# Optimization experiments

Hardware: AMD Instinct MI355X
Metric: run time of the kernel (lower is better)

Reference implementation:

```python
import jax, jax.numpy as jnp
import numpy as np

B = 1048576  # batch size
D = 16       # in_dim == hid_dim == out_dim (required by the torch matmul broadcasting)


def setup_inputs() -> dict:
    key = jax.random.key(0)
    kx, kw = jax.random.split(key)
    x = jax.random.normal(kx, (B, D), dtype=jnp.float32)
    W = jax.random.normal(kw, (D, D, D), dtype=jnp.float32) * (1.0 / D)
    return {"x": x, "W": W}


def reference(x, W):
    # Original torch: xBx = x @ W @ x.T permuted, then take the batch diagonal.
    # Mathematically: out[b, k] = sum_{i, j} x[b, i] * W[k, i, j] * x[b, j]
    # (batched bilinear/quadratic form per output channel k). We compute only
    # the needed diagonal terms instead of the full BxB cross-batch product.
    return jnp.einsum('bi,kij,bj->bk', x, W, x)
```

## Files before the change

kernel.cpp:

```cpp
#include <hip/hip_runtime.h>
#include <hip/hip_bf16.h>


typedef __attribute__((ext_vector_type(8)))  short  short8;
typedef __attribute__((ext_vector_type(8)))  __bf16 bf16x8;
typedef __attribute__((ext_vector_type(4)))  float  floatx4;

#define DEV static __device__ __forceinline__

constexpr int cA(int c) {
    if (c < 24) { const int dIdx = c >> 1, v = c & 1;
        const int hi = dIdx / 3, lo = dIdx % 3 + 1;
        const int base = (hi == 3) ? 1 : 0;
        const int l = v ? ((lo == 1) ? 2 : 1) : 0;
        return base * 4 + l; }
    if (c < 36) { const int g = c - 24, hi = g / 4 + 1, l = g & 3;
        const int base = (hi == 3) ? 1 : 0;
        return base * 4 + l; }
    return c - 36;
}
constexpr int cDd(int c) {
    if (c < 24) { const int dIdx = c >> 1;
        return (dIdx / 3) * 4 + (dIdx % 3 + 1); }
    if (c < 36) { return ((c - 24) / 4 + 1) * 4; }
    return 0;
}
constexpr int   cB(int c) { return cA(c) ^ cDd(c); }
constexpr float cW(int c) { return (c >= 24 && c < 36) ? 0.5f : 1.0f; }

template <int C>
DEV float pval(const float* xv) {
    return xv[cA(C)] * xv[cB(C)];
}

template <int S>
DEV short8 make_afrag(const float* xv) {
    union { short8 s; __hip_bfloat162 h[4]; } u;
    u.h[0] = __float22bfloat162_rn(make_float2(pval<8 * S + 0>(xv), pval<8 * S + 1>(xv)));
    u.h[1] = __float22bfloat162_rn(make_float2(pval<8 * S + 2>(xv), pval<8 * S + 3>(xv)));
    u.h[2] = __float22bfloat162_rn(make_float2(pval<8 * S + 4>(xv), pval<8 * S + 5>(xv)));
    u.h[3] = __float22bfloat162_rn(make_float2(pval<8 * S + 6>(xv), pval<8 * S + 7>(xv)));
    return u.s;
}

DEV floatx4 mfma_bf16(short8 a, short8 b, floatx4 c) {
    return __builtin_amdgcn_mfma_f32_16x16x32_bf16(
        __builtin_bit_cast(bf16x8, a), __builtin_bit_cast(bf16x8, b), c, 0, 0, 0);
}

DEV float q_elem(const float* __restrict__ W, int e) {
    const int n = e / 160;
    const int k = e - n * 160;
    const int s = k >> 5, q = (k >> 3) & 3, j = k & 7;
    const int c = 8 * s + j;
    const int I = cA(c) ^ (q << 2);
    const int J = cB(c) ^ (q << 2);
    return (I == J) ? W[n * 256 + I * 16 + I]
                    : cW(c) * (W[n * 256 + I * 16 + J] + W[n * 256 + J * 16 + I]);
}

__global__ __launch_bounds__(256, 8)
void bilinear16_kernel(const float* __restrict__ x, const float* __restrict__ W,
                       float* __restrict__ out, int ntiles) {
    __shared__ __align__(16) short Qt[16][160];
    __shared__ __align__(16) float Tb[4][320];

    const int tid = threadIdx.x;
    for (int e = tid; e < 16 * 160; e += 256) {
        __hip_bfloat16 h = __float2bfloat16(q_elem(W, e));
        Qt[0][e] = *reinterpret_cast<short*>(&h);
    }
    __syncthreads();

    const int lane = tid & 63;
    const int n    = lane & 15;
    const int q    = lane >> 4;
    float* const tb = Tb[tid >> 6];

    const short8 b0 = *reinterpret_cast<const short8*>(&Qt[n][0 * 32 + q * 8]);
    const short8 b1 = *reinterpret_cast<const short8*>(&Qt[n][1 * 32 + q * 8]);
    const short8 b2 = *reinterpret_cast<const short8*>(&Qt[n][2 * 32 + q * 8]);
    const short8 b3 = *reinterpret_cast<const short8*>(&Qt[n][3 * 32 + q * 8]);
    const short8 b4 = *reinterpret_cast<const short8*>(&Qt[n][4 * 32 + q * 8]);

    const int waveId = blockIdx.x * 4 + (tid >> 6);
    const int nwaves = gridDim.x * 4;

    for (int t = waveId; t < ntiles; t += nwaves) {
        const float4 own = *reinterpret_cast<const float4*>(
            x + (size_t)t * 256 + n * 16 + q * 4);
        float4 s1, s2;
        s1.x = __shfl_xor(own.x, 16); s1.y = __shfl_xor(own.y, 16);
        s1.z = __shfl_xor(own.z, 16); s1.w = __shfl_xor(own.w, 16);
        s2.x = __shfl_xor(own.x, 32); s2.y = __shfl_xor(own.y, 32);
        s2.z = __shfl_xor(own.z, 32); s2.w = __shfl_xor(own.w, 32);
        const float xv[12] = {own.x, own.y, own.z, own.w,
                              s1.x,  s1.y,  s1.z,  s1.w,
                              s2.x,  s2.y,  s2.z,  s2.w};

        floatx4 acc = {0.f, 0.f, 0.f, 0.f};
        acc = mfma_bf16(make_afrag<0>(xv), b0, acc);
        acc = mfma_bf16(make_afrag<1>(xv), b1, acc);
        acc = mfma_bf16(make_afrag<2>(xv), b2, acc);
        acc = mfma_bf16(make_afrag<3>(xv), b3, acc);
        acc = mfma_bf16(make_afrag<4>(xv), b4, acc);

        tb[(q * 4 + 0) * 20 + n] = acc[0];
        tb[(q * 4 + 1) * 20 + n] = acc[1];
        tb[(q * 4 + 2) * 20 + n] = acc[2];
        tb[(q * 4 + 3) * 20 + n] = acc[3];
        const float4 o = *reinterpret_cast<const float4*>(
            &tb[(lane >> 2) * 20 + (lane & 3) * 4]);
        *reinterpret_cast<float4*>(out + (size_t)t * 256 + lane * 4) = o;
    }
}

extern "C" void kernel_launch(void* const* d_in, const int* in_sizes, int n_in,
                              void* d_out, int out_size, void* d_ws, size_t ws_size,
                              hipStream_t stream) {
    const float* x = (const float*)d_in[0];
    const float* W = (const float*)d_in[1];
    float* out = (float*)d_out;
    const int Bn = in_sizes[0] / 16;
    const int ntiles = Bn >> 4;
    bilinear16_kernel<<<2048, 256, 0, stream>>>(x, W, out, ntiles);
}
```

Before: 121.5 us.

## Replace shuffles and LDS transpose with redundant loads and direct scalar stores

Each lane now loads its three needed float4 chunks of x directly from global memory (relying on cache for the redundant reads) instead of exchanging them with cross-lane shuffles. The LDS staging buffer used to transpose the MFMA output into float4 rows is removed, and results are written as four strided scalar stores per lane. The MFMA chain is also split across two accumulators to shorten the dependency chain. This trades shuffle and LDS traffic plus waits for three times the load instructions and less-vectorized, 64-byte-segment output writes.

```diff
diff --git a/kernel.cpp b/kernel.cpp
--- a/kernel.cpp
+++ b/kernel.cpp
@@ -63,7 +63,6 @@
 void bilinear16_kernel(const float* __restrict__ x, const float* __restrict__ W,
                        float* __restrict__ out, int ntiles) {
     __shared__ __align__(16) short Qt[16][160];
-    __shared__ __align__(16) float Tb[4][320];
 
     const int tid = threadIdx.x;
     for (int e = tid; e < 16 * 160; e += 256) {
@@ -75,7 +74,6 @@
     const int lane = tid & 63;
     const int n    = lane & 15;
     const int q    = lane >> 4;
-    float* const tb = Tb[tid >> 6];
 
     const short8 b0 = *reinterpret_cast<const short8*>(&Qt[n][0 * 32 + q * 8]);
     const short8 b1 = *reinterpret_cast<const short8*>(&Qt[n][1 * 32 + q * 8]);
@@ -87,31 +85,28 @@
     const int nwaves = gridDim.x * 4;
 
     for (int t = waveId; t < ntiles; t += nwaves) {
-        const float4 own = *reinterpret_cast<const float4*>(
-            x + (size_t)t * 256 + n * 16 + q * 4);
-        float4 s1, s2;
-        s1.x = __shfl_xor(own.x, 16); s1.y = __shfl_xor(own.y, 16);
-        s1.z = __shfl_xor(own.z, 16); s1.w = __shfl_xor(own.w, 16);
-        s2.x = __shfl_xor(own.x, 32); s2.y = __shfl_xor(own.y, 32);
-        s2.z = __shfl_xor(own.z, 32); s2.w = __shfl_xor(own.w, 32);
-        const float xv[12] = {own.x, own.y, own.z, own.w,
-                              s1.x,  s1.y,  s1.z,  s1.w,
-                              s2.x,  s2.y,  s2.z,  s2.w};
+        const float* xt = x + (size_t)t * 256 + n * 16;
+        const float4 v0 = *reinterpret_cast<const float4*>(xt + q * 4);
+        const float4 v1 = *reinterpret_cast<const float4*>(xt + (q ^ 1) * 4);
+        const float4 v2 = *reinterpret_cast<const float4*>(xt + (q ^ 2) * 4);
+        const float xv[12] = {v0.x, v0.y, v0.z, v0.w,
+                              v1.x, v1.y, v1.z, v1.w,
+                              v2.x, v2.y, v2.z, v2.w};
 
-        floatx4 acc = {0.f, 0.f, 0.f, 0.f};
-        acc = mfma_bf16(make_afrag<0>(xv), b0, acc);
-        acc = mfma_bf16(make_afrag<1>(xv), b1, acc);
-        acc = mfma_bf16(make_afrag<2>(xv), b2, acc);
-        acc = mfma_bf16(make_afrag<3>(xv), b3, acc);
-        acc = mfma_bf16(make_afrag<4>(xv), b4, acc);
+        floatx4 acc0 = {0.f, 0.f, 0.f, 0.f};
+        floatx4 acc1 = {0.f, 0.f, 0.f, 0.f};
+        acc0 = mfma_bf16(make_afrag<0>(xv), b0, acc0);
+        acc1 = mfma_bf16(make_afrag<1>(xv), b1, acc1);
+        acc0 = mfma_bf16(make_afrag<2>(xv), b2, acc0);
+        acc1 = mfma_bf16(make_afrag<3>(xv), b3, acc1);
+        acc0 = mfma_bf16(make_afrag<4>(xv), b4, acc0);
+        acc0 = acc0 + acc1;
 
-        tb[(q * 4 + 0) * 20 + n] = acc[0];
-        tb[(q * 4 + 1) * 20 + n] = acc[1];
-        tb[(q * 4 + 2) * 20 + n] = acc[2];
-        tb[(q * 4 + 3) * 20 + n] = acc[3];
-        const float4 o = *reinterpret_cast<const float4*>(
-            &tb[(lane >> 2) * 20 + (lane & 3) * 4]);
-        *reinterpret_cast<float4*>(out + (size_t)t * 256 + lane * 4) = o;
+        float* ob = out + (size_t)t * 256 + q * 64 + n;
+        ob[0]  = acc0[0];
+        ob[16] = acc0[1];
+        ob[32] = acc0[2];
+        ob[48] = acc0[3];
     }
 }
 
```

New measurement: 137.9 us. 1.14x slower.

## Prefetch x tiles into LDS via async global_load_lds with double-buffered ring

Applied to the files above, without the earlier changes.

When the tile count equals eight per wave, each wave streams its eight tiles through a two-slot LDS ring using global_load_lds. The loads are issued two tiles ahead and waited on with explicit vmcnt, so memory latency overlaps with MFMA compute. A rotated LDS layout replaces the cross-lane shuffles that built the per-row x values. It also swaps the library bf16 conversion for a cheaper add-and-shift pack that does not handle NaN, and pins the B fragments in AGPRs. The path depends on hand-set waitcnt values and a fixed tile count; any other size falls back to the old loop.

```diff
diff --git a/kernel.cpp b/kernel.cpp
--- a/kernel.cpp
+++ b/kernel.cpp
@@ -33,13 +33,19 @@
     return xv[cA(C)] * xv[cB(C)];
 }
 
+DEV unsigned pack_bf16(float a, float b) {
+    const unsigned ua = __builtin_bit_cast(unsigned, a) + 0x8000u;
+    const unsigned ub = __builtin_bit_cast(unsigned, b) + 0x8000u;
+    return (ua >> 16) | (ub & 0xFFFF0000u);
+}
+
 template <int S>
 DEV short8 make_afrag(const float* xv) {
-    union { short8 s; __hip_bfloat162 h[4]; } u;
-    u.h[0] = __float22bfloat162_rn(make_float2(pval<8 * S + 0>(xv), pval<8 * S + 1>(xv)));
-    u.h[1] = __float22bfloat162_rn(make_float2(pval<8 * S + 2>(xv), pval<8 * S + 3>(xv)));
-    u.h[2] = __float22bfloat162_rn(make_float2(pval<8 * S + 4>(xv), pval<8 * S + 5>(xv)));
-    u.h[3] = __float22bfloat162_rn(make_float2(pval<8 * S + 6>(xv), pval<8 * S + 7>(xv)));
+    union { short8 s; unsigned u[4]; } u;
+    u.u[0] = pack_bf16(pval<8 * S + 0>(xv), pval<8 * S + 1>(xv));
+    u.u[1] = pack_bf16(pval<8 * S + 2>(xv), pval<8 * S + 3>(xv));
+    u.u[2] = pack_bf16(pval<8 * S + 4>(xv), pval<8 * S + 5>(xv));
+    u.u[3] = pack_bf16(pval<8 * S + 6>(xv), pval<8 * S + 7>(xv));
     return u.s;
 }
 
@@ -59,11 +65,15 @@
                     : cW(c) * (W[n * 256 + I * 16 + J] + W[n * 256 + J * 16 + I]);
 }
 
+typedef const __attribute__((address_space(1))) unsigned char* gptr_t;
+typedef       __attribute__((address_space(3))) unsigned char* lptr_t;
+
 __global__ __launch_bounds__(256, 8)
 void bilinear16_kernel(const float* __restrict__ x, const float* __restrict__ W,
                        float* __restrict__ out, int ntiles) {
     __shared__ __align__(16) short Qt[16][160];
     __shared__ __align__(16) float Tb[4][320];
+    __shared__ __align__(16) float Ring[4][2][256];
 
     const int tid = threadIdx.x;
     for (int e = tid; e < 16 * 160; e += 256) {
@@ -75,44 +85,96 @@
     const int lane = tid & 63;
     const int n    = lane & 15;
     const int q    = lane >> 4;
-    float* const tb = Tb[tid >> 6];
+    const int wid  = __builtin_amdgcn_readfirstlane(tid >> 6);
+    float* const tb   = Tb[wid];
+    float* const ring = &Ring[wid][0][0];
 
-    const short8 b0 = *reinterpret_cast<const short8*>(&Qt[n][0 * 32 + q * 8]);
-    const short8 b1 = *reinterpret_cast<const short8*>(&Qt[n][1 * 32 + q * 8]);
-    const short8 b2 = *reinterpret_cast<const short8*>(&Qt[n][2 * 32 + q * 8]);
-    const short8 b3 = *reinterpret_cast<const short8*>(&Qt[n][3 * 32 + q * 8]);
-    const short8 b4 = *reinterpret_cast<const short8*>(&Qt[n][4 * 32 + q * 8]);
+    short8 b0 = *reinterpret_cast<const short8*>(&Qt[n][0 * 32 + q * 8]);
+    short8 b1 = *reinterpret_cast<const short8*>(&Qt[n][1 * 32 + q * 8]);
+    short8 b2 = *reinterpret_cast<const short8*>(&Qt[n][2 * 32 + q * 8]);
+    short8 b3 = *reinterpret_cast<const short8*>(&Qt[n][3 * 32 + q * 8]);
+    short8 b4 = *reinterpret_cast<const short8*>(&Qt[n][4 * 32 + q * 8]);
+    asm("" : "+a"(b0)); asm("" : "+a"(b1)); asm("" : "+a"(b2));
+    asm("" : "+a"(b3)); asm("" : "+a"(b4));
 
-    const int waveId = blockIdx.x * 4 + (tid >> 6);
+    const int waveId = blockIdx.x * 4 + wid;
     const int nwaves = gridDim.x * 4;
 
-    for (int t = waveId; t < ntiles; t += nwaves) {
-        const float4 own = *reinterpret_cast<const float4*>(
-            x + (size_t)t * 256 + n * 16 + q * 4);
-        float4 s1, s2;
-        s1.x = __shfl_xor(own.x, 16); s1.y = __shfl_xor(own.y, 16);
-        s1.z = __shfl_xor(own.z, 16); s1.w = __shfl_xor(own.w, 16);
-        s2.x = __shfl_xor(own.x, 32); s2.y = __shfl_xor(own.y, 32);
-        s2.z = __shfl_xor(own.z, 32); s2.w = __shfl_xor(own.w, 32);
-        const float xv[12] = {own.x, own.y, own.z, own.w,
-                              s1.x,  s1.y,  s1.z,  s1.w,
-                              s2.x,  s2.y,  s2.z,  s2.w};
+    const int src_off = (lane >> 2) * 16 + ((((lane & 3) - ((lane >> 3) & 3)) & 3) << 2);
+    const int rotn = ((lane & 15) >> 1) & 3;
+    const int ro0 = n * 16 + (((q       + rotn) & 3) << 2);
+    const int ro1 = n * 16 + ((((q ^ 1) + rotn) & 3) << 2);
+    const int ro2 = n * 16 + ((((q ^ 2) + rotn) & 3) << 2);
 
+    auto tile_compute = [&](const float* rs, float* obase) {
+        const float4 v0 = *reinterpret_cast<const float4*>(rs + ro0);
+        const float4 v1 = *reinterpret_cast<const float4*>(rs + ro1);
+        const float4 v2 = *reinterpret_cast<const float4*>(rs + ro2);
+        const float xv[12] = {v0.x, v0.y, v0.z, v0.w,
+                              v1.x, v1.y, v1.z, v1.w,
+                              v2.x, v2.y, v2.z, v2.w};
         floatx4 acc = {0.f, 0.f, 0.f, 0.f};
         acc = mfma_bf16(make_afrag<0>(xv), b0, acc);
         acc = mfma_bf16(make_afrag<1>(xv), b1, acc);
         acc = mfma_bf16(make_afrag<2>(xv), b2, acc);
         acc = mfma_bf16(make_afrag<3>(xv), b3, acc);
         acc = mfma_bf16(make_afrag<4>(xv), b4, acc);
-
         tb[(q * 4 + 0) * 20 + n] = acc[0];
         tb[(q * 4 + 1) * 20 + n] = acc[1];
         tb[(q * 4 + 2) * 20 + n] = acc[2];
         tb[(q * 4 + 3) * 20 + n] = acc[3];
         const float4 o = *reinterpret_cast<const float4*>(
             &tb[(lane >> 2) * 20 + (lane & 3) * 4]);
-        *reinterpret_cast<float4*>(out + (size_t)t * 256 + lane * 4) = o;
+        *reinterpret_cast<float4*>(obase + lane * 4) = o;
+    };
+
+#define PREF(J)                                                                  \
+    __builtin_amdgcn_global_load_lds(                                            \
+        (gptr_t)(const void*)(x + (size_t)(t0 + (J) * nwaves) * 256 + src_off),  \
+        (lptr_t)(void*)(ring + ((J) & 1) * 256), 16, 0, 0)
+
+#define TILE(J, VMC)                                                             \
+    do {                                                                         \
+        asm volatile("s_waitcnt vmcnt(" #VMC ")" ::: "memory");                  \
+        tile_compute(ring + ((J) & 1) * 256,                                     \
+                     out + (size_t)(t0 + (J) * nwaves) * 256);                   \
+        if ((J) < 6) { asm volatile("" ::: "memory"); PREF((J) + 2); }           \
+    } while (0)
+
+    if (ntiles == nwaves * 8) {
+        const int t0 = waveId;
+        PREF(0); PREF(1);
+        TILE(0, 1); TILE(1, 2); TILE(2, 2); TILE(3, 2);
+        TILE(4, 2); TILE(5, 2); TILE(6, 2); TILE(7, 1);
+    } else {
+        for (int t = waveId; t < ntiles; t += nwaves) {
+            const float4 own = *reinterpret_cast<const float4*>(
+                x + (size_t)t * 256 + n * 16 + q * 4);
+            float4 s1, s2;
+            s1.x = __shfl_xor(own.x, 16); s1.y = __shfl_xor(own.y, 16);
+            s1.z = __shfl_xor(own.z, 16); s1.w = __shfl_xor(own.w, 16);
+            s2.x = __shfl_xor(own.x, 32); s2.y = __shfl_xor(own.y, 32);
+            s2.z = __shfl_xor(own.z, 32); s2.w = __shfl_xor(own.w, 32);
+            const float xv[12] = {own.x, own.y, own.z, own.w,
+                                  s1.x,  s1.y,  s1.z,  s1.w,
+                                  s2.x,  s2.y,  s2.z,  s2.w};
+            floatx4 acc = {0.f, 0.f, 0.f, 0.f};
+            acc = mfma_bf16(make_afrag<0>(xv), b0, acc);
+            acc = mfma_bf16(make_afrag<1>(xv), b1, acc);
+            acc = mfma_bf16(make_afrag<2>(xv), b2, acc);
+            acc = mfma_bf16(make_afrag<3>(xv), b3, acc);
+            acc = mfma_bf16(make_afrag<4>(xv), b4, acc);
+            tb[(q * 4 + 0) * 20 + n] = acc[0];
+            tb[(q * 4 + 1) * 20 + n] = acc[1];
+            tb[(q * 4 + 2) * 20 + n] = acc[2];
+            tb[(q * 4 + 3) * 20 + n] = acc[3];
+            const float4 o = *reinterpret_cast<const float4*>(
+                &tb[(lane >> 2) * 20 + (lane & 3) * 4]);
+            *reinterpret_cast<float4*>(out + (size_t)t * 256 + lane * 4) = o;
+        }
     }
+#undef TILE
+#undef PREF
 }
 
 extern "C" void kernel_launch(void* const* d_in, const int* in_sizes, int n_in,
```

Measured after the change: 122.1 us. No clear change (+0.5%).
